# Kernel optimization log

Measured on AMD Instinct MI355X. Metric: run time of the kernel, lower is better.

Reference implementation:

```python
import jax, jax.numpy as jnp
import numpy as np

S = 24; N = S * S; D = 1024; B = 4; H = 8; HD = D // H; K = 8
LN_EPS = 1e-5


def _spiral_indices(s, clockwise):
    inds = []
    top, bottom, left, right = 0, s - 1, 0, s - 1
    if clockwise:
        while top <= bottom and left <= right:
            for j in range(left, right + 1):
                inds.append((top, j))
            top += 1
            for i in range(top, bottom + 1):
                inds.append((i, right))
            right -= 1
            if top <= bottom:
                for j in range(right, left - 1, -1):
                    inds.append((bottom, j))
                bottom -= 1
            if left <= right:
                for i in range(bottom, top - 1, -1):
                    inds.append((i, left))
                left += 1
    else:
        while top <= bottom and left <= right:
            for i in range(top, bottom + 1):
                inds.append((i, left))
            left += 1
            for j in range(left, right + 1):
                inds.append((bottom, j))
            bottom -= 1
            if left <= right:
                for i in range(bottom, top - 1, -1):
                    inds.append((i, right))
                right -= 1
            if top <= bottom:
                for j in range(right, left - 1, -1):
                    inds.append((top, j))
                top += 1
    return np.array([i * s + j for i, j in inds], dtype=np.int32)


def _diag_indices(s, anti):
    idx = []
    for offset in (range(2 * s - 1) if anti else range(-(s - 1), s)):
        for i in range(s):
            j = (offset - i) if anti else (i + offset)
            if 0 <= j < s:
                idx.append(i * s + j)
    return np.array(idx, dtype=np.int32)


def _build_scan_indices(s):
    # Composite (scan + restore) permutation per direction: out_i = Linear_i(x[:, idx_i])
    ar = np.arange(s * s, dtype=np.int32).reshape(s, s)
    lr = ar.reshape(-1)                      # left_right: identity
    rl_scan = ar[:, ::-1].reshape(-1)        # right_left scan
    rl_restore = ar[:, ::-1].reshape(-1)     # restore flips width back
    rl = rl_scan[rl_restore]                 # composes to identity
    tb = ar.T.reshape(-1)                    # top_bottom (restore is plain view -> no inverse!)
    bt_scan = ar[::-1, :].T.reshape(-1)      # bottom_top scan: flip(transpose) flatten
    bt_restore = ar[::-1, :].reshape(-1)     # restore: view->transpose->flip(2)->transpose
    bt = bt_scan[bt_restore]
    dm = _diag_indices(s, anti=False)        # restore is plain view
    da = _diag_indices(s, anti=True)
    sc = _spiral_indices(s, clockwise=True)
    scc = _spiral_indices(s, clockwise=False)
    return np.stack([lr, rl, tb, bt, dm, da, sc, scc], axis=0)  # [8, N]


def setup_inputs() -> dict:
    key = jax.random.key(0)
    ks = jax.random.split(key, 12)
    sc = D ** -0.5
    return {
        "vision_features": jax.random.normal(ks[0], (B, N, D), dtype=jnp.float32),
        "dir_W": jax.random.normal(ks[1], (K, D, D), dtype=jnp.float32) * sc,
        "dir_b": jax.random.normal(ks[2], (K, D), dtype=jnp.float32) * 0.01,
        "in_proj_w": jax.random.normal(ks[3], (3 * D, D), dtype=jnp.float32) * sc,
        "in_proj_b": jax.random.normal(ks[4], (3 * D,), dtype=jnp.float32) * 0.01,
        "out_proj_w": jax.random.normal(ks[5], (D, D), dtype=jnp.float32) * sc,
        "out_proj_b": jax.random.normal(ks[6], (D,), dtype=jnp.float32) * 0.01,
        "fin_w": jax.random.normal(ks[7], (D, D), dtype=jnp.float32) * sc,
        "fin_b": jax.random.normal(ks[8], (D,), dtype=jnp.float32) * 0.01,
        "ln_g": jnp.ones((D,), dtype=jnp.float32),
        "ln_b": jnp.zeros((D,), dtype=jnp.float32),
        "scan_idx": jnp.asarray(_build_scan_indices(S)),  # [8, N] int32
    }


def reference(vision_features, dir_W, dir_b, in_proj_w, in_proj_b,
              out_proj_w, out_proj_b, fin_w, fin_b, ln_g, ln_b, scan_idx):
    b, n, d = vision_features.shape
    # Fused per-direction gather + batched GEMM: [B,8,N,D]
    gathered = vision_features[:, scan_idx]                     # [B,K,N,D]
    dirs = jnp.einsum('bknd,kde->bkne', gathered, dir_W) + dir_b[None, :, None, :]
    kv = dirs.reshape(b, K * n, d)                              # [B,8N,D]
    # MultiheadAttention (batch_first, 8 heads, eval -> no dropout)
    wq, wk, wv = in_proj_w[:d], in_proj_w[d:2 * d], in_proj_w[2 * d:]
    bq, bk, bv = in_proj_b[:d], in_proj_b[d:2 * d], in_proj_b[2 * d:]
    q = (vision_features @ wq.T + bq).reshape(b, n, H, HD).transpose(0, 2, 1, 3)
    k = (kv @ wk.T + bk).reshape(b, K * n, H, HD).transpose(0, 2, 1, 3)
    v = (kv @ wv.T + bv).reshape(b, K * n, H, HD).transpose(0, 2, 1, 3)
    scores = jnp.einsum('bhnd,bhmd->bhnm', q, k) / jnp.sqrt(jnp.asarray(HD, q.dtype))
    attn = jax.nn.softmax(scores, axis=-1)
    o = jnp.einsum('bhnm,bhmd->bhnd', attn, v).transpose(0, 2, 1, 3).reshape(b, n, d)
    fused = o @ out_proj_w.T + out_proj_b
    # output_projection: Linear -> LayerNorm (dropout inactive)
    y = fused @ fin_w.T + fin_b
    mu = jnp.mean(y, axis=-1, keepdims=True)
    var = jnp.mean(jnp.square(y - mu), axis=-1, keepdims=True)
    y = (y - mu) * jax.lax.rsqrt(var + LN_EPS) * ln_g + ln_b
    return y + vision_features
```

## Files before the change

kernel.cpp:

```cpp
#include <hip/hip_runtime.h>
#include <hip/hip_bf16.h>

typedef __attribute__((ext_vector_type(8))) short short8;
typedef __attribute__((ext_vector_type(4))) float f32x4;
typedef __attribute__((ext_vector_type(4))) int i32x4;

#define NTOK 576
#define DIM  1024
#define NB   4
#define NH   8
#define HD   128
#define KDIR 8
#define KN   4608
#define NSPLIT 4
#define NT 18

__device__ __forceinline__ float us2f(unsigned short u) {
    unsigned int x = ((unsigned int)u) << 16;
    return __uint_as_float(x);
}
__device__ __forceinline__ unsigned short f2us(float f) {
    unsigned int x = __float_as_uint(f);
    unsigned int r = x + 0x7fffu + ((x >> 16) & 1u);
    return (unsigned short)(r >> 16);
}

typedef __attribute__((address_space(3))) unsigned int lds_uint;
typedef const __attribute__((address_space(1))) unsigned int glb_uint;
__device__ __forceinline__ void async16(const unsigned short* g, unsigned short* l) {
    __builtin_amdgcn_global_load_lds((glb_uint*)g, (lds_uint*)l, 16, 0, 0);
}
__device__ __forceinline__ void wait_vm0_barrier() {
    asm volatile("s_waitcnt vmcnt(0)" ::: "memory");
    __builtin_amdgcn_s_barrier();
    __builtin_amdgcn_sched_barrier(0);
}

__global__ void detect_kernel(const unsigned int* __restrict__ src, int* meta)
{
    if (threadIdx.x == 0) {
        int cnt = 0;
        for (int i = 0; i < 256; ++i) {
            unsigned u = src[(long)i * 16384] & 0xFFFFu;
            unsigned e = (u >> 7) & 0xFFu;
            cnt += (e >= 90 && e <= 150) ? 1 : 0;
        }
        meta[0] = (cnt >= 192) ? 1 : 0;
    }
}

struct ConvJobs {
    const void* src[10];
    unsigned short* dst[10];
    int n4[10];
    int bstart[10];
};
__global__ __launch_bounds__(256)
void conv_all(ConvJobs J, const int* __restrict__ meta)
{
    const int b = blockIdx.x;
    int ji = 0;
    #pragma unroll
    for (int i = 1; i < 10; ++i) if (b >= J.bstart[i]) ji = i;
    const long base = (long)(b - J.bstart[ji]) * 1024 + threadIdx.x;
    const long n4 = J.n4[ji];
    if (meta[0]) {
        const ushort4* s = (const ushort4*)J.src[ji];
        ushort4* d = (ushort4*)J.dst[ji];
        #pragma unroll
        for (int t = 0; t < 4; ++t) {
            long i = base + t * 256;
            if (i < n4) d[i] = s[i];
        }
    } else {
        const float4* s = (const float4*)J.src[ji];
        ushort4* d = (ushort4*)J.dst[ji];
        #pragma unroll
        for (int t = 0; t < 4; ++t) {
            long i = base + t * 256;
            if (i < n4) {
                float4 v = s[i];
                ushort4 o;
                o.x = f2us(v.x); o.y = f2us(v.y); o.z = f2us(v.z); o.w = f2us(v.w);
                d[i] = o;
            }
        }
    }
}

__global__ __launch_bounds__(256)
void transpose_conv(const void* __restrict__ src, unsigned short* __restrict__ dst,
                    const int* __restrict__ meta)
{
    const int k = blockIdx.y;
    const int ty = blockIdx.x >> 5, tx = blockIdx.x & 31;
    const int d0 = ty * 32, e0 = tx * 32;
    __shared__ float tl[32][33];
    const int t = threadIdx.x;
    const int row = t >> 3, c4 = (t & 7) * 4;
    const long sbase = ((long)k * 1024 + d0 + row) * 1024 + e0 + c4;
    if (meta[0]) {
        const unsigned short* s = (const unsigned short*)src;
        ushort4 v = *(const ushort4*)(s + sbase);
        tl[row][c4+0] = us2f(v.x); tl[row][c4+1] = us2f(v.y);
        tl[row][c4+2] = us2f(v.z); tl[row][c4+3] = us2f(v.w);
    } else {
        const float* s = (const float*)src;
        float4 v = *(const float4*)(s + sbase);
        tl[row][c4+0] = v.x; tl[row][c4+1] = v.y;
        tl[row][c4+2] = v.z; tl[row][c4+3] = v.w;
    }
    __syncthreads();
    ushort4 o;
    o.x = f2us(tl[c4+0][row]); o.y = f2us(tl[c4+1][row]);
    o.z = f2us(tl[c4+2][row]); o.w = f2us(tl[c4+3][row]);
    *(ushort4*)(dst + ((long)k * 1024 + e0 + row) * 1024 + d0 + c4) = o;
}

template<int MODE, int TN, int BM, int BN>
__global__ __launch_bounds__(256)
void gemm_glds(const unsigned short* __restrict__ A, const unsigned short* __restrict__ Bw,
               const unsigned short* __restrict__ bias, unsigned short* __restrict__ C,
               const unsigned short* __restrict__ B2, const unsigned short* __restrict__ bias2,
               unsigned short* __restrict__ C2,
               int M, long bStride, long biasStride)
{
    constexpr int MI = BM / 32, NI = BN / 32;
    const int z = blockIdx.y;
    const unsigned short* Bb;
    const unsigned short* Gb;
    if constexpr (MODE == 6) {
        Bb = (z < 8) ? Bw + (long)z * bStride : B2;
        Gb = (z < 8) ? bias + (long)z * biasStride : bias2;
    } else {
        Bb = Bw + (long)z * bStride;
        Gb = bias + (long)z * biasStride;
    }
    const int tm = blockIdx.x / TN;
    const int tn = blockIdx.x % TN;

    __shared__ __align__(16) unsigned short As[BM * 64];
    __shared__ __align__(16) unsigned short Bs[BN * 64];

    const int tid = threadIdx.x, lane = tid & 63, wid = tid >> 6;
    const int wm = wid >> 1, wn = wid & 1;
    const int r0 = lane & 15, hi = lane >> 4;
    const int lr = lane >> 3;
    const int lg = lane & 7;

    f32x4 zz = {0.f, 0.f, 0.f, 0.f};
    f32x4 acc[MI][NI];
    #pragma unroll
    for (int i = 0; i < MI; ++i)
        #pragma unroll
        for (int j = 0; j < NI; ++j) acc[i][j] = zz;

    const int sgc = ((lg ^ (lr & 7)) << 3);

    for (int k0 = 0; k0 < 1024; k0 += 64) {
        #pragma unroll
        for (int j = 0; j < BM / 32; ++j) {
            int rb = wid * (BM / 4) + j * 8;
            async16(A + (long)(tm * BM + rb + lr) * 1024 + k0 + sgc, &As[rb * 64]);
        }
        #pragma unroll
        for (int j = 0; j < BN / 32; ++j) {
            int rb = wid * (BN / 4) + j * 8;
            async16(Bb + (long)(tn * BN + rb + lr) * 1024 + k0 + sgc, &Bs[rb * 64]);
        }
        __syncthreads();
        __builtin_amdgcn_s_setprio(1);
        #pragma unroll
        for (int kd = 0; kd < 2; ++kd) {
            const int pg = ((kd * 4 + hi) ^ (r0 & 7)) << 3;
            short8 af[MI], bfr[NI];
            #pragma unroll
            for (int mi = 0; mi < MI; ++mi)
                af[mi] = *reinterpret_cast<const short8*>(&As[(wm * (BM/2) + mi * 16 + r0) * 64 + pg]);
            #pragma unroll
            for (int ni = 0; ni < NI; ++ni)
                bfr[ni] = *reinterpret_cast<const short8*>(&Bs[(wn * (BN/2) + ni * 16 + r0) * 64 + pg]);
            #pragma unroll
            for (int mi = 0; mi < MI; ++mi)
                #pragma unroll
                for (int ni = 0; ni < NI; ++ni)
                    acc[mi][ni] = __builtin_amdgcn_mfma_f32_16x16x32_bf16(af[mi], bfr[ni], acc[mi][ni], 0, 0, 0);
        }
        __builtin_amdgcn_s_setprio(0);
        __syncthreads();
    }

    const float QSCL = 0.08838834764831845f * 1.4426950408889634f;
    const int jr = hi * 4;
    #pragma unroll
    for (int ni = 0; ni < NI; ++ni) {
        int cg = tn * BN + wn * (BN/2) + ni * 16 + r0;
        float bv = us2f(Gb[cg]);
        #pragma unroll
        for (int mi = 0; mi < MI; ++mi) {
            #pragma unroll
            for (int j = 0; j < 4; ++j) {
                int rg = tm * BM + wm * (BM/2) + mi * 16 + jr + j;
                float val = acc[mi][ni][j] + bv;
                if constexpr (MODE == 0) {
                    C[(long)rg * 1024 + cg] = f2us(val);
                } else {
                    int b = rg / 576, n = rg - b * 576;
                    if (z == 8) {
                        int h = cg >> 7, d = cg & 127;
                        C2[((long)(b * 8 + h) * 576 + n) * 128 + d] = f2us(val * QSCL);
                    } else {
                        C[((long)b * 4608 + (long)z * 576 + n) * 1024 + cg] = f2us(val);
                    }
                }
            }
        }
    }
}

__global__ __launch_bounds__(512, 1)
void gemm_kv8(const unsigned short* __restrict__ A, const unsigned short* __restrict__ Bw,
              const unsigned short* __restrict__ bias, unsigned short* __restrict__ Kh,
              unsigned short* __restrict__ VTh)
{
    const int tm = blockIdx.x >> 3;
    const int tn = blockIdx.x & 7;

    __shared__ __align__(16) unsigned short As[2][256 * 64];
    __shared__ __align__(16) unsigned short Bs[2][256 * 64];

    const int tid = threadIdx.x, lane = tid & 63, wid = tid >> 6;
    const int wm = wid >> 2, wn = wid & 3;
    const int r0 = lane & 15, hi = lane >> 4;

    const int srow = tid >> 3;
    const int sgc  = (((tid & 7) ^ (srow & 7)) << 3);
    const long abase = (long)(tm * 256 + srow) * 1024 + sgc;
    const long bbase = (long)(tn * 256 + srow) * 1024 + sgc;
    const int  ldst  = wid * 512;

    f32x4 zz = {0.f, 0.f, 0.f, 0.f};
    f32x4 acc[8][4];
    #pragma unroll
    for (int i = 0; i < 8; ++i)
        #pragma unroll
        for (int j = 0; j < 4; ++j) acc[i][j] = zz;

    auto stageA = [&](int kt, int buf) {
        #pragma unroll
        for (int r = 0; r < 4; ++r)
            async16(A + abase + (long)r * 65536 + kt * 64, &As[buf][r * 4096 + ldst]);
    };
    auto stageB = [&](int kt, int buf) {
        #pragma unroll
        for (int r = 0; r < 4; ++r)
            async16(Bw + bbase + (long)r * 65536 + kt * 64, &Bs[buf][r * 4096 + ldst]);
    };

    stageA(0, 0);
    stageB(0, 0);

    const int arow0 = wm * 128 + r0;
    const int brow0 = wn * 64 + r0;
    const int pg0 = ((hi ^ (r0 & 7)) << 3);
    const int pg1 = (((4 + hi) ^ (r0 & 7)) << 3);

    for (int kt = 0; kt < 16; ++kt) {
        const unsigned short* Ac = As[kt & 1];
        const unsigned short* Bc = Bs[kt & 1];
        __builtin_amdgcn_s_barrier();
        if (kt < 15) {
            stageA(kt + 1, (kt + 1) & 1);
            asm volatile("s_waitcnt vmcnt(4)" ::: "memory");
        } else {
            asm volatile("s_waitcnt vmcnt(0)" ::: "memory");
        }
        __builtin_amdgcn_sched_barrier(0);

        #pragma unroll
        for (int q = 0; q < 4; ++q) {
            if (q == 1 && kt < 15) stageB(kt + 1, (kt + 1) & 1);
            short8 af[2][2], bf[4][2];
            #pragma unroll
            for (int dm = 0; dm < 2; ++dm) {
                const int row = (arow0 + (q * 2 + dm) * 16) * 64;
                af[dm][0] = *reinterpret_cast<const short8*>(&Ac[row + pg0]);
                af[dm][1] = *reinterpret_cast<const short8*>(&Ac[row + pg1]);
            }
            #pragma unroll
            for (int ni = 0; ni < 4; ++ni) {
                const int row = (brow0 + ni * 16) * 64;
                bf[ni][0] = *reinterpret_cast<const short8*>(&Bc[row + pg0]);
                bf[ni][1] = *reinterpret_cast<const short8*>(&Bc[row + pg1]);
            }
            __builtin_amdgcn_s_setprio(1);
            #pragma unroll
            for (int dm = 0; dm < 2; ++dm)
                #pragma unroll
                for (int ni = 0; ni < 4; ++ni) {
                    acc[q*2+dm][ni] = __builtin_amdgcn_mfma_f32_16x16x32_bf16(af[dm][0], bf[ni][0], acc[q*2+dm][ni], 0, 0, 0);
                    acc[q*2+dm][ni] = __builtin_amdgcn_mfma_f32_16x16x32_bf16(af[dm][1], bf[ni][1], acc[q*2+dm][ni], 0, 0, 0);
                }
            __builtin_amdgcn_s_setprio(0);
            __builtin_amdgcn_sched_barrier(0);
        }
    }

    const int jr = hi * 4;
    if (tn < 4) {
        #pragma unroll
        for (int ni = 0; ni < 4; ++ni) {
            int cg = tn * 256 + wn * 64 + ni * 16 + r0;
            float bv = us2f(bias[cg]);
            int h = cg >> 7, d = cg & 127;
            #pragma unroll
            for (int mi = 0; mi < 8; ++mi) {
                #pragma unroll
                for (int j = 0; j < 4; ++j) {
                    int rg = tm * 256 + wm * 128 + mi * 16 + jr + j;
                    int b = rg / 4608, kv = rg - b * 4608;
                    Kh[((long)(b * 8 + h) * 4608 + kv) * 128 + d] = f2us(acc[mi][ni][j] + bv);
                }
            }
        }
    } else {
        #pragma unroll
        for (int ni = 0; ni < 4; ++ni) {
            int cgr = tn * 256 + wn * 64 + ni * 16 + r0;
            float bv = us2f(bias[cgr]);
            int cg = cgr - 1024;
            int h = cg >> 7, d = cg & 127;
            #pragma unroll
            for (int mi = 0; mi < 8; ++mi) {
                int rgb = tm * 256 + wm * 128 + mi * 16 + jr;
                int b = rgb / 4608, kv = rgb - b * 4608;
                int r = kv & 63;
                int P = ((r >> 5) & 1) * 32 + ((r >> 3) & 1) * 16 + ((r >> 2) & 1) * 8
                      + ((r >> 4) & 1) * 4 + (r & 3);
                ushort4 o;
                o.x = f2us(acc[mi][ni][0] + bv);
                o.y = f2us(acc[mi][ni][1] + bv);
                o.z = f2us(acc[mi][ni][2] + bv);
                o.w = f2us(acc[mi][ni][3] + bv);
                *(ushort4*)&VTh[((long)(b * 8 + h) * 128 + d) * 4608 + (kv & ~63) + P] = o;
            }
        }
    }
}

__global__ __launch_bounds__(256, 2)
void attn_kernel7(const unsigned short* __restrict__ Qh, const unsigned short* __restrict__ Kh,
                  const unsigned short* __restrict__ VTh, unsigned short* __restrict__ Opart,
                  float2* __restrict__ Ml)
{
    const int bid = blockIdx.x;
    const int logical = (bid & 7) * 48 + (bid >> 3);
    const int bhsp = logical / 3;
    const int qt = logical - bhsp * 3;
    const int bh = bhsp >> 2;
    const int sp = bhsp & 3;

    const int tid = threadIdx.x;
    const int lane = tid & 63, wid = tid >> 6;
    const int r0 = lane & 15, hi = lane >> 4;

    __shared__ __align__(16) unsigned short Ks[2][64 * 128];
    __shared__ __align__(16) unsigned short VT[2][128 * 64];

    short8 qf[3][4];
    #pragma unroll
    for (int c = 0; c < 3; ++c) {
        const long qoff = ((long)bh * NTOK + qt * 192 + c * 64 + wid * 16 + r0) * HD + hi * 8;
        #pragma unroll
        for (int kd = 0; kd < 4; ++kd)
            qf[c][kd] = *reinterpret_cast<const short8*>(Qh + qoff + kd * 32);
    }

    f32x4 zz = {0.f, 0.f, 0.f, 0.f};
    f32x4 oacc[3][8];
    #pragma unroll
    for (int c = 0; c < 3; ++c)
        #pragma unroll
        for (int i = 0; i < 8; ++i) oacc[c][i] = zz;
    float mrun[3], lrun[3];
    #pragma unroll
    for (int c = 0; c < 3; ++c) { mrun[c] = -1e30f; lrun[c] = 0.f; }

    int offK[4], offV[4];
    #pragma unroll
    for (int j = 0; j < 4; ++j) {
        offK[j] = (wid * 16 + 4 * j + hi) * 128 + (((lane & 15) ^ ((4 * j + hi) & 7)) << 3);
        offV[j] = (wid * 32 + 8 * j + (lane >> 3)) * KN + (((lane & 7) ^ (lane >> 3)) << 3);
    }
    const unsigned short* kp = Kh + (long)bh * KN * HD + (long)(sp * (KN / NSPLIT)) * HD;
    const unsigned short* vp = VTh + (long)bh * HD * KN + sp * (KN / NSPLIT);

    auto stage = [&](int buf) {
        #pragma unroll
        for (int j = 0; j < 4; ++j) {
            async16(kp + offK[j], &Ks[buf][(wid * 16 + 4 * j) * 128]);
            async16(vp + offV[j], &VT[buf][(wid * 32 + 8 * j) * 64]);
        }
    };

    stage(0);
    for (int kt = 0; kt < NT; ++kt) {
        wait_vm0_barrier();
        if (kt < NT - 1) { kp += 64 * HD; vp += 64; stage((kt + 1) & 1); }
        const unsigned short* Ksb = Ks[kt & 1];
        const unsigned short* VTb = VT[kt & 1];

        f32x4 s[3][4];
        #pragma unroll
        for (int c = 0; c < 3; ++c)
            #pragma unroll
            for (int nb = 0; nb < 4; ++nb) s[c][nb] = zz;
        __builtin_amdgcn_s_setprio(1);
        #pragma unroll
        for (int nb = 0; nb < 4; ++nb) {
            #pragma unroll
            for (int kd = 0; kd < 4; ++kd) {
                short8 kf = *reinterpret_cast<const short8*>(
                    &Ksb[(nb * 16 + r0) * 128 + (((kd * 4 + hi) ^ (r0 & 7)) << 3)]);
                s[0][nb] = __builtin_amdgcn_mfma_f32_16x16x32_bf16(kf, qf[0][kd], s[0][nb], 0, 0, 0);
                s[1][nb] = __builtin_amdgcn_mfma_f32_16x16x32_bf16(kf, qf[1][kd], s[1][nb], 0, 0, 0);
                s[2][nb] = __builtin_amdgcn_mfma_f32_16x16x32_bf16(kf, qf[2][kd], s[2][nb], 0, 0, 0);
            }
        }
        __builtin_amdgcn_s_setprio(0);

        unsigned pk0[3][4], pk1[3][4];
        #pragma unroll
        for (int c = 0; c < 3; ++c) {
            float mt = fmaxf(fmaxf(fmaxf(s[c][0][0], s[c][0][1]), fmaxf(s[c][0][2], s[c][0][3])),
                       fmaxf(fmaxf(fmaxf(s[c][1][0], s[c][1][1]), fmaxf(s[c][1][2], s[c][1][3])),
                       fmaxf(fmaxf(fmaxf(s[c][2][0], s[c][2][1]), fmaxf(s[c][2][2], s[c][2][3])),
                             fmaxf(fmaxf(s[c][3][0], s[c][3][1]), fmaxf(s[c][3][2], s[c][3][3])))));
            if (!__all(mt - mrun[c] <= 8.0f)) {
                float mr = fmaxf(mt, __shfl_xor(mt, 16));
                mr = fmaxf(mr, __shfl_xor(mr, 32));
                float mn = fmaxf(mrun[c], mr);
                float scl = exp2f(mrun[c] - mn);
                mrun[c] = mn;
                lrun[c] *= scl;
                #pragma unroll
                for (int db = 0; db < 8; ++db)
                    #pragma unroll
                    for (int j = 0; j < 4; ++j)
                        oacc[c][db][j] *= scl;
            }
            float rt = 0.f;
            #pragma unroll
            for (int nb = 0; nb < 4; ++nb)
                #pragma unroll
                for (int j = 0; j < 4; ++j) {
                    s[c][nb][j] = exp2f(s[c][nb][j] - mrun[c]);
                    rt += s[c][nb][j];
                }
            lrun[c] += rt;
            #pragma unroll
            for (int nb = 0; nb < 4; ++nb) {
                asm("v_cvt_pk_bf16_f32 %0, %1, %2" : "=v"(pk0[c][nb]) : "v"(s[c][nb][0]), "v"(s[c][nb][1]));
                asm("v_cvt_pk_bf16_f32 %0, %1, %2" : "=v"(pk1[c][nb]) : "v"(s[c][nb][2]), "v"(s[c][nb][3]));
            }
        }

        __builtin_amdgcn_s_setprio(1);
        #pragma unroll
        for (int kd = 0; kd < 2; ++kd) {
            short8 pf[3];
            #pragma unroll
            for (int c = 0; c < 3; ++c) {
                i32x4 fr;
                fr[0] = (int)pk0[c][2 * kd];
                fr[1] = (int)pk1[c][2 * kd];
                fr[2] = (int)pk0[c][2 * kd + 1];
                fr[3] = (int)pk1[c][2 * kd + 1];
                pf[c] = *reinterpret_cast<short8*>(&fr);
            }
            #pragma unroll
            for (int db = 0; db < 8; ++db) {
                short8 vf = *reinterpret_cast<const short8*>(
                    &VTb[(db * 16 + r0) * 64 + (((kd * 4 + hi) ^ (r0 & 7)) << 3)]);
                oacc[0][db] = __builtin_amdgcn_mfma_f32_16x16x32_bf16(vf, pf[0], oacc[0][db], 0, 0, 0);
                oacc[1][db] = __builtin_amdgcn_mfma_f32_16x16x32_bf16(vf, pf[1], oacc[1][db], 0, 0, 0);
                oacc[2][db] = __builtin_amdgcn_mfma_f32_16x16x32_bf16(vf, pf[2], oacc[2][db], 0, 0, 0);
            }
        }
        __builtin_amdgcn_s_setprio(0);
    }

    #pragma unroll
    for (int c = 0; c < 3; ++c) {
        float lr = lrun[c];
        lr += __shfl_xor(lr, 16);
        lr += __shfl_xor(lr, 32);
        const float inv = 1.f / lr;
        const long po = ((long)(sp * 32 + bh) * NTOK + qt * 192 + c * 64 + wid * 16 + r0) * HD;
        #pragma unroll
        for (int db = 0; db < 8; ++db) {
            ushort4 o;
            o.x = f2us(oacc[c][db][0] * inv);
            o.y = f2us(oacc[c][db][1] * inv);
            o.z = f2us(oacc[c][db][2] * inv);
            o.w = f2us(oacc[c][db][3] * inv);
            *(ushort4*)&Opart[po + db * 16 + hi * 4] = o;
        }
        if (lane < 16) {
            const long mo = (long)(sp * 32 + bh) * NTOK + qt * 192 + c * 64 + wid * 16 + r0;
            Ml[mo] = make_float2(mrun[c], lr);
        }
    }
}

__global__ __launch_bounds__(256)
void attn_reduce(const unsigned short* __restrict__ Opart, const float2* __restrict__ Ml,
                 unsigned short* __restrict__ Ob)
{
    const int qt = blockIdx.x, bh = blockIdx.y;
    const int t = threadIdx.x;
    const int rl = t >> 2, dc = (t & 3) * 32;
    const int q = qt * 64 + rl;

    float m[NSPLIT], l[NSPLIT];
    float M = -1e30f;
    #pragma unroll
    for (int sp = 0; sp < NSPLIT; ++sp) {
        float2 v = Ml[(long)(sp * 32 + bh) * NTOK + q];
        m[sp] = v.x; l[sp] = v.y;
        M = fmaxf(M, v.x);
    }
    float w[NSPLIT], denom = 0.f;
    #pragma unroll
    for (int sp = 0; sp < NSPLIT; ++sp) {
        w[sp] = l[sp] * exp2f(m[sp] - M);
        denom += w[sp];
    }
    const float inv = 1.f / denom;
    const int b = bh >> 3, h = bh & 7;
    #pragma unroll
    for (int dj = 0; dj < 4; ++dj) {
        float a[8];
        #pragma unroll
        for (int e = 0; e < 8; ++e) a[e] = 0.f;
        #pragma unroll
        for (int sp = 0; sp < NSPLIT; ++sp) {
            short8 v = *reinterpret_cast<const short8*>(
                &Opart[((long)(sp * 32 + bh) * NTOK + q) * HD + dc + dj * 8]);
            #pragma unroll
            for (int e = 0; e < 8; ++e)
                a[e] += w[sp] * us2f((unsigned short)v[e]);
        }
        short8 o;
        #pragma unroll
        for (int e = 0; e < 8; ++e) o[e] = (short)f2us(a[e] * inv);
        *reinterpret_cast<short8*>(&Ob[((long)b * NTOK + q) * 1024 + h * 128 + dc + dj * 8]) = o;
    }
}

__global__ __launch_bounds__(256)
void ln2_kernel(const unsigned short* __restrict__ Y, const unsigned short* __restrict__ g,
                const unsigned short* __restrict__ be, const unsigned short* __restrict__ vis,
                void* __restrict__ dout, const int* __restrict__ meta)
{
    const int row = blockIdx.x;
    const int tid = threadIdx.x;
    const int lane = tid & 63, wid = tid >> 6;
    const unsigned short* yr = Y + (long)row * DIM;
    ushort4 raw = reinterpret_cast<const ushort4*>(yr)[tid];
    float v[4];
    v[0] = us2f(raw.x); v[1] = us2f(raw.y); v[2] = us2f(raw.z); v[3] = us2f(raw.w);
    float s1 = 0.f, s2 = 0.f;
    #pragma unroll
    for (int i = 0; i < 4; ++i) { s1 += v[i]; s2 += v[i] * v[i]; }
    #pragma unroll
    for (int off = 1; off < 64; off <<= 1) {
        s1 += __shfl_xor(s1, off);
        s2 += __shfl_xor(s2, off);
    }
    __shared__ float red[2][4];
    if (lane == 0) { red[0][wid] = s1; red[1][wid] = s2; }
    __syncthreads();
    s1 = red[0][0] + red[0][1] + red[0][2] + red[0][3];
    s2 = red[1][0] + red[1][1] + red[1][2] + red[1][3];
    const float mu = s1 * (1.f / DIM);
    const float var = s2 * (1.f / DIM) - mu * mu;
    const float inv = rsqrtf(var + 1e-5f);
    ushort4 gg = reinterpret_cast<const ushort4*>(g)[tid];
    ushort4 bb = reinterpret_cast<const ushort4*>(be)[tid];
    ushort4 vv = reinterpret_cast<const ushort4*>(vis + (long)row * DIM)[tid];
    float o0 = (v[0] - mu) * inv * us2f(gg.x) + us2f(bb.x) + us2f(vv.x);
    float o1 = (v[1] - mu) * inv * us2f(gg.y) + us2f(bb.y) + us2f(vv.y);
    float o2 = (v[2] - mu) * inv * us2f(gg.z) + us2f(bb.z) + us2f(vv.z);
    float o3 = (v[3] - mu) * inv * us2f(gg.w) + us2f(bb.w) + us2f(vv.w);
    if (meta[0]) {
        ushort4 o;
        o.x = f2us(o0); o.y = f2us(o1); o.z = f2us(o2); o.w = f2us(o3);
        reinterpret_cast<ushort4*>((unsigned short*)dout + (long)row * DIM)[tid] = o;
    } else {
        float4 o = make_float4(o0, o1, o2, o3);
        reinterpret_cast<float4*>((float*)dout + (long)row * DIM)[tid] = o;
    }
}

extern "C" void kernel_launch(void* const* d_in, const int* in_sizes, int n_in,
                              void* d_out, int out_size, void* d_ws, size_t ws_size,
                              hipStream_t stream)
{
    unsigned long long w = (unsigned long long)d_ws;
    int* meta = (int*)w; w += 256;

    const int cidx[10] = {0, 2, 3, 4, 5, 6, 7, 8, 9, 10};
    const long csz[10] = {
        (long)NB * NTOK * DIM,
        (long)KDIR * DIM,
        3L * DIM * DIM,
        3L * DIM,
        (long)DIM * DIM,
        DIM,
        (long)DIM * DIM,
        DIM, DIM, DIM
    };
    unsigned short* cv[10];
    for (int i = 0; i < 10; ++i) {
        cv[i] = (unsigned short*)w;
        w += (csz[i] * 2 + 255) & ~255ULL;
    }
    unsigned short* dWT = (unsigned short*)w; w += (long)KDIR * DIM * DIM * 2;

    const size_t big = (size_t)NB * KDIR * NTOK * DIM * 2;
    const size_t sml = (size_t)NB * NTOK * DIM * 2;
    unsigned short* dirs = (unsigned short*)w; w += big;
    unsigned short* Kh   = (unsigned short*)w; w += big;
    unsigned short* VTh  = (unsigned short*)w; w += big;
    unsigned short* Qh   = (unsigned short*)w; w += sml;
    unsigned short* Ob   = (unsigned short*)w; w += sml;
    unsigned short* Fu   = (unsigned short*)w; w += sml;
    unsigned short* Y2   = (unsigned short*)w; w += sml;
    float2* Ml = (float2*)w; w += (long)NSPLIT * 32 * NTOK * sizeof(float2);
    unsigned short* Opart = dirs;

    const unsigned short* vision = cv[0];
    const unsigned short* dirb = cv[1];
    const unsigned short* inW = cv[2];
    const unsigned short* inB = cv[3];
    const unsigned short* outW = cv[4];
    const unsigned short* outB = cv[5];
    const unsigned short* finW = cv[6];
    const unsigned short* finB = cv[7];
    const unsigned short* lng = cv[8];
    const unsigned short* lnbt = cv[9];

    dim3 blk(256, 1, 1);

    detect_kernel<<<dim3(1), dim3(64), 0, stream>>>((const unsigned int*)d_in[1], meta);

    ConvJobs J;
    int bacc = 0;
    for (int i = 0; i < 10; ++i) {
        J.src[i] = d_in[cidx[i]];
        J.dst[i] = cv[i];
        J.n4[i] = (int)(csz[i] / 4);
        J.bstart[i] = bacc;
        bacc += (int)((csz[i] / 4 + 1023) / 1024);
    }
    conv_all<<<dim3(bacc), blk, 0, stream>>>(J, meta);
    transpose_conv<<<dim3(1024, KDIR), blk, 0, stream>>>(d_in[1], dWT, meta);

    gemm_glds<6, 8, 128, 128><<<dim3(18 * 8, 9), blk, 0, stream>>>(
        vision, dWT, dirb, dirs, inW, inB, Qh, NB * NTOK, (long)DIM * DIM, DIM);

    gemm_kv8<<<dim3(72 * 8), dim3(512), 0, stream>>>(
        dirs, inW + DIM * DIM, inB + DIM, Kh, VTh);

    attn_kernel7<<<dim3(3 * 32 * NSPLIT), blk, 0, stream>>>(Qh, Kh, VTh, Opart, Ml);

    attn_reduce<<<dim3(9, 32), blk, 0, stream>>>(Opart, Ml, Ob);

    gemm_glds<0, 16, 64, 64><<<dim3(36 * 16, 1), blk, 0, stream>>>(
        Ob, outW, outB, Fu, nullptr, nullptr, nullptr, NB * NTOK, 0L, 0L);

    gemm_glds<0, 16, 64, 64><<<dim3(36 * 16, 1), blk, 0, stream>>>(
        Fu, finW, finB, Y2, nullptr, nullptr, nullptr, NB * NTOK, 0L, 0L);

    ln2_kernel<<<dim3(NB * NTOK), blk, 0, stream>>>(Y2, lng, lnbt, vision, d_out, meta);
}
```

Measured before the change: 366.0 us.

## Restructure K/V projection GEMM into 8-slot half-tile LDS pipeline

Replaces the double-buffered A/B staging in the K/V projection GEMM with a single 128KB LDS ring of eight 128-row half-tile slots. Loads for the next k-steps are issued one half-tile at a time, interleaved with each MFMA phase, so more global loads stay in flight across barriers. B fragments are loaded once per k-step and reused across four A sub-phases. The schedule adds a workgroup barrier after every phase and depends on intricate vmcnt accounting, so a slot-reuse ordering mistake would corrupt results, and the extra barriers may offset the deeper prefetch.

Result: faster. 344.1 us (-6.0%).

```diff
diff --git a/kernel.cpp b/kernel.cpp
--- a/kernel.cpp
+++ b/kernel.cpp
@@ -219,25 +219,39 @@
 }
 
 __global__ __launch_bounds__(512, 1)
-void gemm_kv8(const unsigned short* __restrict__ A, const unsigned short* __restrict__ Bw,
-              const unsigned short* __restrict__ bias, unsigned short* __restrict__ Kh,
-              unsigned short* __restrict__ VTh)
+void gemm_kv8p(const unsigned short* __restrict__ A, const unsigned short* __restrict__ Bw,
+               const unsigned short* __restrict__ bias, unsigned short* __restrict__ Kh,
+               unsigned short* __restrict__ VTh)
 {
     const int tm = blockIdx.x >> 3;
     const int tn = blockIdx.x & 7;
-
-    __shared__ __align__(16) unsigned short As[2][256 * 64];
-    __shared__ __align__(16) unsigned short Bs[2][256 * 64];
+    __shared__ __align__(16) unsigned short Hs[8 * 8192];
 
     const int tid = threadIdx.x, lane = tid & 63, wid = tid >> 6;
     const int wm = wid >> 2, wn = wid & 3;
     const int r0 = lane & 15, hi = lane >> 4;
 
-    const int srow = tid >> 3;
-    const int sgc  = (((tid & 7) ^ (srow & 7)) << 3);
-    const long abase = (long)(tm * 256 + srow) * 1024 + sgc;
-    const long bbase = (long)(tn * 256 + srow) * 1024 + sgc;
-    const int  ldst  = wid * 512;
+    const int srow0 = tid >> 3;
+    const int sg = tid & 7;
+    const int dst0 = srow0 * 64 + sg * 8;
+    const int sc0 = ((sg ^ (srow0 & 7)) << 3);
+
+    auto stageHalf = [&](int slot, const unsigned short* src) {
+        async16(src + (long)srow0 * 1024 + sc0, &Hs[slot * 8192 + dst0]);
+        async16(src + (long)(srow0 + 64) * 1024 + sc0, &Hs[slot * 8192 + dst0 + 4096]);
+    };
+
+    const unsigned short* Abase = A + (long)(tm * 256) * 1024;
+    const unsigned short* Bbase = Bw + (long)(tn * 256) * 1024;
+
+    stageHalf(0, Bbase);
+    stageHalf(1, Bbase + 131072);
+    stageHalf(2, Abase);
+    stageHalf(3, Abase + 131072);
+    stageHalf(4, Bbase + 64);
+    stageHalf(5, Bbase + 131072 + 64);
+    asm volatile("s_waitcnt vmcnt(0)" ::: "memory");
+    __builtin_amdgcn_s_barrier();
 
     f32x4 zz = {0.f, 0.f, 0.f, 0.f};
     f32x4 acc[8][4];
@@ -246,63 +260,69 @@
         #pragma unroll
         for (int j = 0; j < 4; ++j) acc[i][j] = zz;
 
-    auto stageA = [&](int kt, int buf) {
-        #pragma unroll
-        for (int r = 0; r < 4; ++r)
-            async16(A + abase + (long)r * 65536 + kt * 64, &As[buf][r * 4096 + ldst]);
-    };
-    auto stageB = [&](int kt, int buf) {
-        #pragma unroll
-        for (int r = 0; r < 4; ++r)
-            async16(Bw + bbase + (long)r * 65536 + kt * 64, &Bs[buf][r * 4096 + ldst]);
-    };
-
-    stageA(0, 0);
-    stageB(0, 0);
-
-    const int arow0 = wm * 128 + r0;
-    const int brow0 = wn * 64 + r0;
-    const int pg0 = ((hi ^ (r0 & 7)) << 3);
-    const int pg1 = (((4 + hi) ^ (r0 & 7)) << 3);
-
-    for (int kt = 0; kt < 16; ++kt) {
-        const unsigned short* Ac = As[kt & 1];
-        const unsigned short* Bc = Bs[kt & 1];
-        __builtin_amdgcn_s_barrier();
-        if (kt < 15) {
-            stageA(kt + 1, (kt + 1) & 1);
-            asm volatile("s_waitcnt vmcnt(4)" ::: "memory");
-        } else {
-            asm volatile("s_waitcnt vmcnt(0)" ::: "memory");
-        }
-        __builtin_amdgcn_sched_barrier(0);
-
-        #pragma unroll
-        for (int q = 0; q < 4; ++q) {
-            if (q == 1 && kt < 15) stageB(kt + 1, (kt + 1) & 1);
-            short8 af[2][2], bf[4][2];
-            #pragma unroll
-            for (int dm = 0; dm < 2; ++dm) {
-                const int row = (arow0 + (q * 2 + dm) * 16) * 64;
-                af[dm][0] = *reinterpret_cast<const short8*>(&Ac[row + pg0]);
-                af[dm][1] = *reinterpret_cast<const short8*>(&Ac[row + pg1]);
-            }
-            #pragma unroll
-            for (int ni = 0; ni < 4; ++ni) {
-                const int row = (brow0 + ni * 16) * 64;
-                bf[ni][0] = *reinterpret_cast<const short8*>(&Bc[row + pg0]);
-                bf[ni][1] = *reinterpret_cast<const short8*>(&Bc[row + pg1]);
-            }
-            __builtin_amdgcn_s_setprio(1);
-            #pragma unroll
-            for (int dm = 0; dm < 2; ++dm)
+    const int pg0 = ((hi) ^ (r0 & 7)) << 3;
+    const int pg1 = ((4 + hi) ^ (r0 & 7)) << 3;
+
+    for (int j = 0; j < 8; ++j) {
+        const unsigned short* Ao  = Abase + (2 * j + 1) * 64;
+        const unsigned short* An  = Abase + (2 * j + 2) * 64;
+        const unsigned short* Bn  = Bbase + (2 * j + 2) * 64;
+        const unsigned short* Bo2 = Bbase + (2 * j + 3) * 64;
+        #pragma unroll
+        for (int kt2 = 0; kt2 < 2; ++kt2) {
+            const int sb = kt2 * 4;
+            short8 bf[4][2];
+            #pragma unroll
+            for (int q = 0; q < 4; ++q) {
+                if (q == 0) {
+                    #pragma unroll
+                    for (int ni = 0; ni < 4; ++ni) {
+                        const unsigned short* bsl =
+                            &Hs[(sb + (wn >> 1)) * 8192 + ((wn & 1) * 64 + ni * 16 + r0) * 64];
+                        bf[ni][0] = *(const short8*)(bsl + pg0);
+                        bf[ni][1] = *(const short8*)(bsl + pg1);
+                    }
+                }
+                short8 af[2][2];
                 #pragma unroll
-                for (int ni = 0; ni < 4; ++ni) {
-                    acc[q*2+dm][ni] = __builtin_amdgcn_mfma_f32_16x16x32_bf16(af[dm][0], bf[ni][0], acc[q*2+dm][ni], 0, 0, 0);
-                    acc[q*2+dm][ni] = __builtin_amdgcn_mfma_f32_16x16x32_bf16(af[dm][1], bf[ni][1], acc[q*2+dm][ni], 0, 0, 0);
+                for (int dm = 0; dm < 2; ++dm) {
+                    const unsigned short* asl =
+                        &Hs[(sb + 2 + wm) * 8192 + ((2 * q + dm) * 16 + r0) * 64];
+                    af[dm][0] = *(const short8*)(asl + pg0);
+                    af[dm][1] = *(const short8*)(asl + pg1);
                 }
-            __builtin_amdgcn_s_setprio(0);
-            __builtin_amdgcn_sched_barrier(0);
+                const int ph = kt2 * 4 + q;
+                if (ph == 0) { stageHalf(6, Ao); stageHalf(7, Ao + 131072); }
+                else if (j < 7) {
+                    if (ph == 1) stageHalf(0, Bn);
+                    else if (ph == 2) stageHalf(1, Bn + 131072);
+                    else if (ph == 4) stageHalf(2, An);
+                    else if (ph == 5) stageHalf(3, An + 131072);
+                    else if (ph == 6) stageHalf(4, Bo2);
+                    else if (ph == 7) stageHalf(5, Bo2 + 131072);
+                }
+                __builtin_amdgcn_sched_barrier(0);
+                __builtin_amdgcn_s_barrier();
+                asm volatile("s_waitcnt lgkmcnt(0)" ::: "memory");
+                __builtin_amdgcn_sched_barrier(0);
+                __builtin_amdgcn_s_setprio(1);
+                #pragma unroll
+                for (int dm = 0; dm < 2; ++dm)
+                    #pragma unroll
+                    for (int ni = 0; ni < 4; ++ni) {
+                        acc[2*q+dm][ni] = __builtin_amdgcn_mfma_f32_16x16x32_bf16(af[dm][0], bf[ni][0], acc[2*q+dm][ni], 0, 0, 0);
+                        acc[2*q+dm][ni] = __builtin_amdgcn_mfma_f32_16x16x32_bf16(af[dm][1], bf[ni][1], acc[2*q+dm][ni], 0, 0, 0);
+                    }
+                __builtin_amdgcn_s_setprio(0);
+                __builtin_amdgcn_sched_barrier(0);
+                if (ph == 3) {
+                    if (j < 7) asm volatile("s_waitcnt vmcnt(4)" ::: "memory");
+                    else       asm volatile("s_waitcnt vmcnt(0)" ::: "memory");
+                } else if (ph == 7 && j < 7) {
+                    asm volatile("s_waitcnt vmcnt(4)" ::: "memory");
+                }
+                __builtin_amdgcn_s_barrier();
+            }
         }
     }
 
@@ -670,7 +690,7 @@
     gemm_glds<6, 8, 128, 128><<<dim3(18 * 8, 9), blk, 0, stream>>>(
         vision, dWT, dirb, dirs, inW, inB, Qh, NB * NTOK, (long)DIM * DIM, DIM);
 
-    gemm_kv8<<<dim3(72 * 8), dim3(512), 0, stream>>>(
+    gemm_kv8p<<<dim3(72 * 8), dim3(512), 0, stream>>>(
         dirs, inW + DIM * DIM, inB + DIM, Kh, VTh);
 
     attn_kernel7<<<dim3(3 * 32 * NSPLIT), blk, 0, stream>>>(Qh, Kh, VTh, Opart, Ml);
```
